# Kernel tuning notes

Hardware: AMD Instinct MI355X
Metric: run time of the kernel (lower is better)

Reference implementation:

```python
import jax, jax.numpy as jnp
import numpy as np

B, S, E, H = 2, 2048, 2048, 16
D = E // H  # 128


def setup_inputs() -> dict:
    key = jax.random.key(0)
    k0, k1, k2, k3 = jax.random.split(key, 4)
    x = jax.random.normal(k0, (B, S, E), dtype=jnp.float32)
    W_in = jax.random.normal(k1, (3 * E, E), dtype=jnp.float32) * 0.02
    b_in = jnp.zeros((3 * E,), dtype=jnp.float32)
    W_out = jax.random.normal(k2, (E, E), dtype=jnp.float32) * 0.02
    b_out = jnp.zeros((E,), dtype=jnp.float32)
    mask = jax.random.randint(k3, (B, S), 0, 2).astype(bool)  # True => masked out
    return {"x": x, "W_in": W_in, "b_in": b_in, "W_out": W_out, "b_out": b_out, "mask": mask}


def reference(x, W_in, b_in, W_out, b_out, mask):
    # fused QKV projection (torch Linear: y = x @ W^T + b)
    qkv = jnp.einsum('bse,fe->bsf', x, W_in) + b_in          # [B,S,3E]
    q, k, v = jnp.split(qkv, 3, axis=-1)
    q = q.reshape(B, S, H, D)
    k = k.reshape(B, S, H, D)
    v = v.reshape(B, S, H, D)
    scale = 1.0 / np.sqrt(D).astype(np.float32)
    scores = jnp.einsum('blhd,bshd->bhls', q, k) * scale     # [B,H,S,S]
    # 2D padding mask: True -> -inf additive bias, broadcast over heads/queries
    bias = jnp.where(mask[:, None, None, :], -jnp.inf, 0.0).astype(scores.dtype)
    attn = jax.nn.softmax(scores + bias, axis=-1)
    ctx = jnp.einsum('bhls,bshd->blhd', attn, v).reshape(B, S, E)
    out = jnp.einsum('ble,fe->blf', ctx, W_out) + b_out      # [B,S,E]
    return out
```

## Files before the change

kernel.cpp:

```cpp
#include <hip/hip_runtime.h>
#include <hip/hip_bf16.h>


typedef __bf16 bf16;
typedef __bf16 bf16x8 __attribute__((ext_vector_type(8)));
typedef __bf16 bf16x4 __attribute__((ext_vector_type(4)));
typedef float  f32x4  __attribute__((ext_vector_type(4)));
typedef float  f32x16 __attribute__((ext_vector_type(16)));

#define LOG2E 1.4426950408889634074f
#define SM_SCALE 0.08838834764831843f

#if defined(__has_builtin)
#if __has_builtin(__builtin_amdgcn_exp2f)
#define EXP2(x) __builtin_amdgcn_exp2f(x)
#else
#define EXP2(x) exp2f(x)
#endif
#else
#define EXP2(x) exp2f(x)
#endif

#define GLOAD_LDS16(gp, lp)                                                    \
  __builtin_amdgcn_global_load_lds(                                           \
      (__attribute__((address_space(1))) void*)(gp),                          \
      (__attribute__((address_space(3))) void*)(lp), 16, 0, 0)

__device__ inline unsigned int cvtpk_bf16(float lo, float hi) {
  unsigned int r;
  asm("v_cvt_pk_bf16_f32 %0, %1, %2" : "=v"(r) : "v"(lo), "v"(hi));
  return r;
}
__device__ inline void plane32_swap(unsigned int& a, unsigned int& b) {
  asm volatile("v_permlane32_swap_b32 %0, %1" : "+v"(a), "+v"(b));
}

__global__ void mask_bias_kernel(const unsigned char* __restrict__ mraw,
                                 float* __restrict__ kbias) {
  __shared__ int f1, f23, f84;
  if (threadIdx.x == 0) { f1 = 0; f23 = 0; f84 = 0; }
  __syncthreads();
  int a1 = 0, a23 = 0, a84 = 0;
  for (int i = threadIdx.x; i < 4096; i += blockDim.x) {
    unsigned char v = mraw[i];
    if (v) {
      int m4 = i & 3;
      if (m4 == 1) a1 = 1;
      else if (m4 >= 2) a23 = 1;
      else if ((i & 7) == 4) a84 = 1;
    }
  }
  if (a1) f1 = 1;
  if (a23) f23 = 1;
  if (a84) f84 = 1;
  __syncthreads();
  const bool isByte = (f1 != 0);
  const bool isF32 = !isByte && (f23 != 0);
  const bool isI32 = !isByte && !isF32 && (f84 != 0);
  for (int i = threadIdx.x; i < 4096; i += blockDim.x) {
    int m;
    if (isByte)      m = (mraw[i] != 0);
    else if (isF32)  m = (((const float*)mraw)[i] != 0.0f);
    else if (isI32)  m = (((const int*)mraw)[i] != 0);
    else             m = (((const long long*)mraw)[i] != 0LL);
    kbias[i] = m ? -30000.0f : 0.0f;
  }
}

__global__ void cvt_f32_bf16_kernel(const float* __restrict__ in,
                                    bf16* __restrict__ out, int n8) {
  int i = blockIdx.x * blockDim.x + threadIdx.x;
  if (i >= n8) return;
  const float4* p = (const float4*)in + (size_t)i * 2;
  float4 a = p[0], c = p[1];
  bf16x8 v;
  v[0] = (bf16)a.x; v[1] = (bf16)a.y; v[2] = (bf16)a.z; v[3] = (bf16)a.w;
  v[4] = (bf16)c.x; v[5] = (bf16)c.y; v[6] = (bf16)c.z; v[7] = (bf16)c.w;
  *((bf16x8*)out + i) = v;
}

template <int EPI>
__global__ __launch_bounds__(256, 2) void gemm_nt(
    const bf16* __restrict__ A, const bf16* __restrict__ B,
    const float* __restrict__ bias, void* __restrict__ Cout,
    bf16* __restrict__ vt, int M, int N, int K) {
  const int lane = threadIdx.x & 63;
  const int w = threadIdx.x >> 6;
  const int wr = w >> 1, wc = w & 1;
  const int l15 = lane & 15, lg = lane >> 4;

  const int nwg = gridDim.x;
  const int cpx = nwg >> 3;
  const int bid = blockIdx.x;
  const int swz = (bid & 7) * cpx + (bid >> 3);
  const int mtiles = M >> 7;
  const int mt = swz % mtiles, nt = swz / mtiles;
  const int m0 = mt << 7, n0 = nt << 7;

  __shared__ __align__(16) unsigned char smem[32768];
  unsigned char* sA = smem;
  unsigned char* sB = smem + 16384;

  const f32x4 Z4 = {0.f, 0.f, 0.f, 0.f};
  f32x4 acc[4][4];
#pragma unroll
  for (int i = 0; i < 4; i++)
#pragma unroll
    for (int j = 0; j < 4; j++) acc[i][j] = Z4;

  const int chunkbase = w * 1024 + lane * 16;

  for (int kt = 0; kt < K; kt += 64) {
#pragma unroll
    for (int c = 0; c < 4; c++) {
      int p = c * 4096 + chunkbase;
      int row = p >> 7, off = p & 127;
      int sb = off ^ ((row & 7) << 4);
      GLOAD_LDS16(A + (size_t)(m0 + row) * K + kt + (sb >> 1),
                  sA + c * 4096 + w * 1024);
      GLOAD_LDS16(B + (size_t)(n0 + row) * K + kt + (sb >> 1),
                  sB + c * 4096 + w * 1024);
    }
    __syncthreads();
#pragma unroll
    for (int ks = 0; ks < 2; ks++) {
      bf16x8 af[4], bfr[4];
#pragma unroll
      for (int i = 0; i < 4; i++) {
        int ar = wr * 64 + i * 16 + l15;
        af[i] = *(const bf16x8*)(sA + ar * 128 +
                                 ((ks * 64 + lg * 16) ^ ((ar & 7) << 4)));
        int br = wc * 64 + i * 16 + l15;
        bfr[i] = *(const bf16x8*)(sB + br * 128 +
                                  ((ks * 64 + lg * 16) ^ ((br & 7) << 4)));
      }
#pragma unroll
      for (int i = 0; i < 4; i++)
#pragma unroll
        for (int j = 0; j < 4; j++)
          acc[i][j] = __builtin_amdgcn_mfma_f32_16x16x32_bf16(
              af[i], bfr[j], acc[i][j], 0, 0, 0);
    }
    __syncthreads();
  }

#pragma unroll
  for (int i = 0; i < 4; i++) {
#pragma unroll
    for (int j = 0; j < 4; j++) {
      const int row0 = m0 + wr * 64 + i * 16 + lg * 4;
      const int col = n0 + wc * 64 + j * 16 + l15;
      const float bv = bias[col];
      f32x4 v = acc[i][j];
#pragma unroll
      for (int r = 0; r < 4; r++) v[r] += bv;
      if (EPI == 0) {
        float* Cf = (float*)Cout;
#pragma unroll
        for (int r = 0; r < 4; r++)
          Cf[(size_t)(row0 + r) * N + col] = v[r];
      } else {
        bf16* Cb = (bf16*)Cout;
        if (col < 4096) {
#pragma unroll
          for (int r = 0; r < 4; r++)
            Cb[(size_t)(row0 + r) * 6144 + col] = (bf16)v[r];
        } else {
          int dg = col - 4096;
          int hh = dg >> 7, dd = dg & 127;
          int bb = row0 >> 11, ss = row0 & 2047;
          bf16x4 pk;
#pragma unroll
          for (int r = 0; r < 4; r++) pk[r] = (bf16)v[r];
          *(bf16x4*)(vt + (size_t)((bb * 16 + hh) * 128 + dd) * 2048 + ss) = pk;
        }
      }
    }
  }
}

__global__ __launch_bounds__(512, 2) void attn_kernel(
    const bf16* __restrict__ qkv, const bf16* __restrict__ vt,
    const float* __restrict__ kbias, bf16* __restrict__ ctx) {
  const int tid = threadIdx.x;
  const int lane = tid & 63;
  const int w = tid >> 6;
  const int l31 = lane & 31;
  const int hb = lane >> 5;
  const int qt = blockIdx.x, h = blockIdx.y, b = blockIdx.z;

  __shared__ __align__(16) unsigned char smem[65536];

  const int qrow0 = qt * 256 + w * 32;
  const size_t tokbase = (size_t)b * 2048;
  const size_t vtbase = (size_t)((b * 16 + h) * 128) * 2048;
  const float* biasb = kbias + b * 2048;
  const float Cmul = SM_SCALE * LOG2E;

  auto stage = [&](int t, int bufsel) {
    const int kv0 = t * 64;
    unsigned char* base = smem + bufsel * 32768;
#pragma unroll
    for (int c = 0; c < 2; c++) {
      int p = c * 8192 + tid * 16;
      int rowk = p >> 8, offk = p & 255;
      int sbk = offk ^ ((rowk & 15) << 4);
      GLOAD_LDS16(qkv + (tokbase + kv0 + rowk) * 6144 + 2048 + h * 128 +
                      (sbk >> 1),
                  base + c * 8192 + w * 1024);
      int rowv = p >> 7, offv = p & 127;
      int sbv = offv ^ ((rowv & 7) << 4);
      GLOAD_LDS16(vt + vtbase + (size_t)rowv * 2048 + kv0 + (sbv >> 1),
                  base + 16384 + c * 8192 + w * 1024);
    }
  };

  stage(0, 0);

  bf16x8 qf[8];
#pragma unroll
  for (int ds = 0; ds < 8; ds++)
    qf[ds] = *(const bf16x8*)(qkv + (tokbase + qrow0 + l31) * 6144 + h * 128 +
                              ds * 16 + hb * 8);

  const f32x16 Z16 = {0.f, 0.f, 0.f, 0.f, 0.f, 0.f, 0.f, 0.f,
                      0.f, 0.f, 0.f, 0.f, 0.f, 0.f, 0.f, 0.f};
  f32x16 opv[4];
#pragma unroll
  for (int d0 = 0; d0 < 4; d0++) opv[d0] = Z16;
  float mrun = -15000.0f, lrun = 0.0f;

  __syncthreads();

  for (int t = 0; t < 32; t++) {
    const int buf = t & 1;
    const int kv0 = t * 64;
    if (t < 31) stage(t + 1, buf ^ 1);
    unsigned char* sK = smem + buf * 32768;
    unsigned char* sVT = sK + 16384;

    f32x4 bb[2][2][2];
#pragma unroll
    for (int kb = 0; kb < 2; kb++)
#pragma unroll
      for (int sb = 0; sb < 2; sb++)
#pragma unroll
        for (int g = 0; g < 2; g++)
          bb[kb][sb][g] = *(const f32x4*)(biasb + kv0 + kb * 32 + sb * 16 +
                                          g * 8 + 4 * hb);

    f32x16 accs[2];
    accs[0] = Z16; accs[1] = Z16;
    __builtin_amdgcn_s_setprio(1);
#pragma unroll
    for (int ds = 0; ds < 8; ds++) {
#pragma unroll
      for (int kb = 0; kb < 2; kb++) {
        int row = kb * 32 + l31;
        bf16x8 kf = *(const bf16x8*)(
            sK + row * 256 + ((ds * 32 + hb * 16) ^ ((row & 15) << 4)));
        accs[kb] = __builtin_amdgcn_mfma_f32_32x32x16_bf16(kf, qf[ds],
                                                           accs[kb], 0, 0, 0);
      }
    }
    __builtin_amdgcn_s_setprio(0);

#pragma unroll
    for (int kb = 0; kb < 2; kb++)
#pragma unroll
      for (int r = 0; r < 16; r++)
        accs[kb][r] =
            accs[kb][r] * Cmul + bb[kb][r >> 3][(r >> 2) & 1][r & 3];

    float vmax = accs[0][0];
#pragma unroll
    for (int kb = 0; kb < 2; kb++)
#pragma unroll
      for (int r = 0; r < 16; r++) vmax = fmaxf(vmax, accs[kb][r]);
    vmax = fmaxf(vmax, __shfl_xor(vmax, 32));

    if (__any(vmax > mrun + 8.0f)) {
      float mnew = fmaxf(mrun, vmax);
      float corr = EXP2(mrun - mnew);
      mrun = mnew;
      lrun *= corr;
#pragma unroll
      for (int r = 0; r < 16; r++) {
        float cv = __shfl(corr, (r & 3) + 8 * (r >> 2) + 4 * hb);
#pragma unroll
        for (int d0 = 0; d0 < 4; d0++) opv[d0][r] *= cv;
      }
    }

    float vsum = 0.0f;
#pragma unroll
    for (int kb = 0; kb < 2; kb++)
#pragma unroll
      for (int r = 0; r < 16; r++) {
        float p = EXP2(accs[kb][r] - mrun);
        accs[kb][r] = p;
        vsum += p;
      }
    vsum += __shfl_xor(vsum, 32);
    lrun += vsum;

    union { unsigned int w4[4]; bf16x8 v; } paf[4];
#pragma unroll
    for (int kb = 0; kb < 2; kb++)
#pragma unroll
      for (int sb = 0; sb < 2; sb++) {
        int r0 = sb * 8;
        unsigned int a0 = cvtpk_bf16(accs[kb][r0 + 0], accs[kb][r0 + 1]);
        unsigned int a1 = cvtpk_bf16(accs[kb][r0 + 2], accs[kb][r0 + 3]);
        unsigned int c0 = cvtpk_bf16(accs[kb][r0 + 4], accs[kb][r0 + 5]);
        unsigned int c1 = cvtpk_bf16(accs[kb][r0 + 6], accs[kb][r0 + 7]);
        plane32_swap(a0, c0);
        plane32_swap(a1, c1);
        int ks = kb * 2 + sb;
        paf[ks].w4[0] = a0; paf[ks].w4[1] = a1;
        paf[ks].w4[2] = c0; paf[ks].w4[3] = c1;
      }

    __builtin_amdgcn_s_setprio(1);
#pragma unroll
    for (int ks = 0; ks < 4; ks++) {
#pragma unroll
      for (int d0 = 0; d0 < 4; d0++) {
        int row = d0 * 32 + l31;
        bf16x8 vf = *(const bf16x8*)(
            sVT + row * 128 + ((ks * 32 + hb * 16) ^ ((row & 7) << 4)));
        opv[d0] = __builtin_amdgcn_mfma_f32_32x32x16_bf16(paf[ks].v, vf,
                                                          opv[d0], 0, 0, 0);
      }
    }
    __builtin_amdgcn_s_setprio(0);

    __syncthreads();
  }

  float linv = 1.0f / lrun;
#pragma unroll
  for (int r = 0; r < 16; r++) {
    float lv = __shfl(linv, (r & 3) + 8 * (r >> 2) + 4 * hb);
    int row = qrow0 + (r & 3) + 8 * (r >> 2) + 4 * hb;
#pragma unroll
    for (int d0 = 0; d0 < 4; d0++)
      ctx[(tokbase + row) * 2048 + h * 128 + d0 * 32 + l31] =
          (bf16)(opv[d0][r] * lv);
  }
}

extern "C" void kernel_launch(void* const* d_in, const int* in_sizes, int n_in,
                              void* d_out, int out_size, void* d_ws,
                              size_t ws_size, hipStream_t stream) {
  const float* x     = (const float*)d_in[0];
  const float* W_in  = (const float*)d_in[1];
  const float* b_in  = (const float*)d_in[2];
  const float* W_out = (const float*)d_in[3];
  const float* b_out = (const float*)d_in[4];
  const unsigned char* mask = (const unsigned char*)d_in[5];
  (void)in_sizes; (void)n_in; (void)out_size; (void)ws_size;

  char* ws = (char*)d_ws;
  bf16* xb    = (bf16*)(ws + 0);
  bf16* wib   = (bf16*)(ws + 16777216);
  bf16* wob   = (bf16*)(ws + 41943040);
  bf16* qkv   = (bf16*)(ws + 50331648);
  bf16* vt    = (bf16*)(ws + 100663296);
  bf16* ctx   = (bf16*)(ws + 117440512);
  float* kbias = (float*)(ws + 134217728);

  mask_bias_kernel<<<1, 1024, 0, stream>>>(mask, kbias);
  cvt_f32_bf16_kernel<<<4096, 256, 0, stream>>>(x, xb, 1048576);
  cvt_f32_bf16_kernel<<<6144, 256, 0, stream>>>(W_in, wib, 1572864);
  cvt_f32_bf16_kernel<<<2048, 256, 0, stream>>>(W_out, wob, 524288);
  gemm_nt<1><<<1536, 256, 0, stream>>>(xb, wib, b_in, (void*)qkv, vt, 4096,
                                       6144, 2048);
  attn_kernel<<<dim3(8, 16, 2), 512, 0, stream>>>(qkv, vt, kbias, ctx);
  gemm_nt<0><<<512, 256, 0, stream>>>(ctx, wob, b_out, d_out, (bf16*)nullptr,
                                      4096, 2048, 2048);
}
```

Measured before the change: 252.3 us.

## Add 256x256-tile QKV GEMM kernel with 8 waves and staged double buffering

Adds a new GEMM kernel for the QKV projection that uses 256x256 output tiles, 512 threads and a 128KB LDS double buffer. A and B tile loads are spread across the four sub-phases of each K step, with setprio raised around the MFMA blocks. Larger tiles raise data reuse per LDS load and cut global traffic. In exchange the grid shrinks to 384 workgroups on 256 CUs, which gives an uneven wave tail, and the large LDS footprint limits occupancy to one block per CU.

Result: slower. 270.8 us (+7.3%).

```diff
diff --git a/kernel.cpp b/kernel.cpp
--- a/kernel.cpp
+++ b/kernel.cpp
@@ -80,6 +80,158 @@
 }
 
 template <int EPI>
+__global__ __launch_bounds__(512, 2) void gemm256(
+    const bf16* __restrict__ A, const bf16* __restrict__ B,
+    const float* __restrict__ bias, void* __restrict__ Cout,
+    bf16* __restrict__ vt, int M, int N, int K) {
+  const int tid = threadIdx.x;
+  const int lane = tid & 63;
+  const int w = tid >> 6;
+  const int wm = w >> 2, wn = w & 3;
+  const int l15 = lane & 15, lg = lane >> 4;
+
+  const int nwg = gridDim.x;
+  const int cpx = nwg >> 3;
+  const int bid = blockIdx.x;
+  const int swz = (bid & 7) * cpx + (bid >> 3);
+  const int mtiles = M >> 8;
+  const int mt = swz % mtiles, ntl = swz / mtiles;
+  const int m0 = mt << 8, n0 = ntl << 8;
+
+  __shared__ __align__(16) unsigned char smem[131072];
+  const int NT = K >> 6;
+
+  auto stageA = [&](int t, int half) {
+    int base = (t & 1) * 32768 + half * 16384;
+#pragma unroll
+    for (int i = 0; i < 2; i++) {
+      int p = i * 8192 + tid * 16;
+      int row = p >> 7, off = p & 127;
+      int sb = off ^ ((row & 7) << 4);
+      GLOAD_LDS16(A + (size_t)(m0 + half * 128 + row) * K + t * 64 + (sb >> 1),
+                  smem + base + i * 8192 + w * 1024);
+    }
+  };
+  auto stageB = [&](int t, int half) {
+    int base = 65536 + (t & 1) * 32768 + half * 16384;
+#pragma unroll
+    for (int i = 0; i < 2; i++) {
+      int p = i * 8192 + tid * 16;
+      int row = p >> 7, off = p & 127;
+      int sb = off ^ ((row & 7) << 4);
+      GLOAD_LDS16(B + (size_t)(n0 + half * 128 + row) * K + t * 64 + (sb >> 1),
+                  smem + base + i * 8192 + w * 1024);
+    }
+  };
+
+  const f32x4 Z4 = {0.f, 0.f, 0.f, 0.f};
+  f32x4 acc[8][4];
+#pragma unroll
+  for (int i = 0; i < 8; i++)
+#pragma unroll
+    for (int j = 0; j < 4; j++) acc[i][j] = Z4;
+
+  stageA(0, 0); stageA(0, 1); stageB(0, 0); stageB(0, 1);
+  stageB(1, 0); stageB(1, 1);
+  asm volatile("s_waitcnt vmcnt(4)" ::: "memory");
+  __builtin_amdgcn_sched_barrier(0);
+  __builtin_amdgcn_s_barrier();
+
+  for (int t = 0; t < NT; t++) {
+    const int abase = (t & 1) * 32768;
+    const int bbase = 65536 + (t & 1) * 32768;
+    bf16x8 bfr[4][2];
+#pragma unroll
+    for (int p = 0; p < 4; p++) {
+      bf16x8 af[2][2];
+#pragma unroll
+      for (int i = 0; i < 2; i++) {
+        int ar = wm * 128 + (2 * p + i) * 16 + l15;
+#pragma unroll
+        for (int ks = 0; ks < 2; ks++)
+          af[i][ks] = *(const bf16x8*)(
+              smem + abase + ar * 128 + ((ks * 64 + lg * 16) ^ ((ar & 7) << 4)));
+      }
+      if (p == 0) {
+#pragma unroll
+        for (int nj = 0; nj < 4; nj++) {
+          int br = wn * 64 + nj * 16 + l15;
+#pragma unroll
+          for (int ks = 0; ks < 2; ks++)
+            bfr[nj][ks] = *(const bf16x8*)(
+                smem + bbase + br * 128 +
+                ((ks * 64 + lg * 16) ^ ((br & 7) << 4)));
+        }
+      }
+      if (p == 0 && t + 1 < NT) stageA(t + 1, 0);
+      if (p == 1 && t + 1 < NT) stageA(t + 1, 1);
+      if (p == 2 && t + 2 < NT) stageB(t + 2, 0);
+      if (p == 3 && t + 2 < NT) stageB(t + 2, 1);
+
+      __builtin_amdgcn_sched_barrier(0);
+      __builtin_amdgcn_s_barrier();
+      asm volatile("s_waitcnt lgkmcnt(0)" ::: "memory");
+      __builtin_amdgcn_sched_barrier(0);
+
+      __builtin_amdgcn_s_setprio(1);
+#pragma unroll
+      for (int i = 0; i < 2; i++)
+#pragma unroll
+        for (int nj = 0; nj < 4; nj++)
+#pragma unroll
+          for (int ks = 0; ks < 2; ks++)
+            acc[2 * p + i][nj] = __builtin_amdgcn_mfma_f32_16x16x32_bf16(
+                af[i][ks], bfr[nj][ks], acc[2 * p + i][nj], 0, 0, 0);
+      __builtin_amdgcn_s_setprio(0);
+
+      if (p == 3) {
+        if (t + 2 < NT) {
+          asm volatile("s_waitcnt vmcnt(4)" ::: "memory");
+        } else if (t + 1 < NT) {
+          asm volatile("s_waitcnt vmcnt(0)" ::: "memory");
+        }
+      }
+      __builtin_amdgcn_sched_barrier(0);
+      __builtin_amdgcn_s_barrier();
+    }
+  }
+
+#pragma unroll
+  for (int mi = 0; mi < 8; mi++) {
+#pragma unroll
+    for (int nj = 0; nj < 4; nj++) {
+      const int row0 = m0 + wm * 128 + mi * 16 + lg * 4;
+      const int col = n0 + wn * 64 + nj * 16 + l15;
+      const float bv = bias[col];
+      f32x4 v = acc[mi][nj];
+#pragma unroll
+      for (int r = 0; r < 4; r++) v[r] += bv;
+      if (EPI == 0) {
+        float* Cf = (float*)Cout;
+#pragma unroll
+        for (int r = 0; r < 4; r++)
+          Cf[(size_t)(row0 + r) * N + col] = v[r];
+      } else {
+        bf16* Cb = (bf16*)Cout;
+        if (col < 4096) {
+#pragma unroll
+          for (int r = 0; r < 4; r++)
+            Cb[(size_t)(row0 + r) * 6144 + col] = (bf16)v[r];
+        } else {
+          int dg = col - 4096;
+          int hh = dg >> 7, dd = dg & 127;
+          int bb = row0 >> 11, ss = row0 & 2047;
+          bf16x4 pk;
+#pragma unroll
+          for (int r = 0; r < 4; r++) pk[r] = (bf16)v[r];
+          *(bf16x4*)(vt + (size_t)((bb * 16 + hh) * 128 + dd) * 2048 + ss) = pk;
+        }
+      }
+    }
+  }
+}
+
+template <int EPI>
 __global__ __launch_bounds__(256, 2) void gemm_nt(
     const bf16* __restrict__ A, const bf16* __restrict__ B,
     const float* __restrict__ bias, void* __restrict__ Cout,
@@ -374,8 +526,8 @@
   cvt_f32_bf16_kernel<<<4096, 256, 0, stream>>>(x, xb, 1048576);
   cvt_f32_bf16_kernel<<<6144, 256, 0, stream>>>(W_in, wib, 1572864);
   cvt_f32_bf16_kernel<<<2048, 256, 0, stream>>>(W_out, wob, 524288);
-  gemm_nt<1><<<1536, 256, 0, stream>>>(xb, wib, b_in, (void*)qkv, vt, 4096,
-                                       6144, 2048);
+  gemm256<1><<<384, 512, 0, stream>>>(xb, wib, b_in, (void*)qkv, vt, 4096,
+                                      6144, 2048);
   attn_kernel<<<dim3(8, 16, 2), 512, 0, stream>>>(qkv, vt, kbias, ctx);
   gemm_nt<0><<<512, 256, 0, stream>>>(ctx, wob, b_out, d_out, (bf16*)nullptr,
                                       4096, 2048, 2048);
```

## Rewrite GEMM as 128x256 tile with multi-buffered async LDS pipeline

Applied to the files above, without the earlier changes.

Replaces the 128x128 single-buffered GEMM with a 512-thread, 128x256-tile kernel. A is double-buffered and B triple-buffered in a 128KB LDS region, and global-to-LDS loads for future k-steps are issued while MFMAs run. The work is split into two half-phases with explicit waitcnt, barriers and setprio to overlap memory with compute. The change is meant to hide load latency behind the synchronous load-then-compute loop and raise reuse per block. In exchange, 128KB of LDS limits occupancy to one block per CU, and the hand-tuned waitcnt counts are fragile.

Measured after the change: 258.3 us. 2.4% more time.

```diff
diff --git a/kernel.cpp b/kernel.cpp
--- a/kernel.cpp
+++ b/kernel.cpp
@@ -80,13 +80,14 @@
 }
 
 template <int EPI>
-__global__ __launch_bounds__(256, 2) void gemm_nt(
+__global__ __launch_bounds__(512, 2) void gemm_wide(
     const bf16* __restrict__ A, const bf16* __restrict__ B,
     const float* __restrict__ bias, void* __restrict__ Cout,
     bf16* __restrict__ vt, int M, int N, int K) {
-  const int lane = threadIdx.x & 63;
-  const int w = threadIdx.x >> 6;
-  const int wr = w >> 1, wc = w & 1;
+  const int tid = threadIdx.x;
+  const int lane = tid & 63;
+  const int w = tid >> 6;
+  const int wm = w >> 2, wn = w & 3;
   const int l15 = lane & 15, lg = lane >> 4;
 
   const int nwg = gridDim.x;
@@ -94,12 +95,34 @@
   const int bid = blockIdx.x;
   const int swz = (bid & 7) * cpx + (bid >> 3);
   const int mtiles = M >> 7;
-  const int mt = swz % mtiles, nt = swz / mtiles;
-  const int m0 = mt << 7, n0 = nt << 7;
-
-  __shared__ __align__(16) unsigned char smem[32768];
-  unsigned char* sA = smem;
-  unsigned char* sB = smem + 16384;
+  const int mt = swz % mtiles, ntl = swz / mtiles;
+  const int m0 = mt << 7, n0 = ntl << 8;
+
+  __shared__ __align__(16) unsigned char smem[131072];
+  const int NT = K >> 6;
+
+  auto stageA = [&](int t) {
+    int base = (t & 1) * 16384;
+#pragma unroll
+    for (int i = 0; i < 2; i++) {
+      int p = i * 8192 + tid * 16;
+      int row = p >> 7, off = p & 127;
+      int sb = off ^ ((row & 7) << 4);
+      GLOAD_LDS16(A + (size_t)(m0 + row) * K + t * 64 + (sb >> 1),
+                  smem + base + i * 8192 + w * 1024);
+    }
+  };
+  auto stageB2 = [&](int t, int i0) {
+    int base = 32768 + (t % 3) * 32768;
+#pragma unroll
+    for (int i = 0; i < 2; i++) {
+      int p = (i0 + i) * 8192 + tid * 16;
+      int row = p >> 7, off = p & 127;
+      int sb = off ^ ((row & 7) << 4);
+      GLOAD_LDS16(B + (size_t)(n0 + row) * K + t * 64 + (sb >> 1),
+                  smem + base + (i0 + i) * 8192 + w * 1024);
+    }
+  };
 
   const f32x4 Z4 = {0.f, 0.f, 0.f, 0.f};
   f32x4 acc[4][4];
@@ -108,50 +131,94 @@
 #pragma unroll
     for (int j = 0; j < 4; j++) acc[i][j] = Z4;
 
-  const int chunkbase = w * 1024 + lane * 16;
-
-  for (int kt = 0; kt < K; kt += 64) {
-#pragma unroll
-    for (int c = 0; c < 4; c++) {
-      int p = c * 4096 + chunkbase;
-      int row = p >> 7, off = p & 127;
-      int sb = off ^ ((row & 7) << 4);
-      GLOAD_LDS16(A + (size_t)(m0 + row) * K + kt + (sb >> 1),
-                  sA + c * 4096 + w * 1024);
-      GLOAD_LDS16(B + (size_t)(n0 + row) * K + kt + (sb >> 1),
-                  sB + c * 4096 + w * 1024);
-    }
-    __syncthreads();
-#pragma unroll
-    for (int ks = 0; ks < 2; ks++) {
-      bf16x8 af[4], bfr[4];
-#pragma unroll
-      for (int i = 0; i < 4; i++) {
-        int ar = wr * 64 + i * 16 + l15;
-        af[i] = *(const bf16x8*)(sA + ar * 128 +
-                                 ((ks * 64 + lg * 16) ^ ((ar & 7) << 4)));
-        int br = wc * 64 + i * 16 + l15;
-        bfr[i] = *(const bf16x8*)(sB + br * 128 +
-                                  ((ks * 64 + lg * 16) ^ ((br & 7) << 4)));
-      }
-#pragma unroll
-      for (int i = 0; i < 4; i++)
-#pragma unroll
-        for (int j = 0; j < 4; j++)
-          acc[i][j] = __builtin_amdgcn_mfma_f32_16x16x32_bf16(
-              af[i], bfr[j], acc[i][j], 0, 0, 0);
-    }
-    __syncthreads();
-  }
-
-#pragma unroll
-  for (int i = 0; i < 4; i++) {
-#pragma unroll
-    for (int j = 0; j < 4; j++) {
-      const int row0 = m0 + wr * 64 + i * 16 + lg * 4;
-      const int col = n0 + wc * 64 + j * 16 + l15;
+  stageA(0); stageB2(0, 0); stageB2(0, 2); stageB2(1, 0); stageB2(1, 2);
+  asm volatile("s_waitcnt vmcnt(4)" ::: "memory");
+  __builtin_amdgcn_sched_barrier(0);
+  __builtin_amdgcn_s_barrier();
+
+  for (int t = 0; t < NT; t++) {
+    const int abase = (t & 1) * 16384;
+    const int bbase = 32768 + (t % 3) * 32768;
+    bf16x8 bfr[4][2];
+
+    bf16x8 af0[2][2];
+#pragma unroll
+    for (int i = 0; i < 2; i++) {
+      int ar = wm * 64 + i * 16 + l15;
+#pragma unroll
+      for (int ks = 0; ks < 2; ks++)
+        af0[i][ks] = *(const bf16x8*)(
+            smem + abase + ar * 128 + ((ks * 64 + lg * 16) ^ ((ar & 7) << 4)));
+    }
+#pragma unroll
+    for (int nj = 0; nj < 4; nj++) {
+      int br = wn * 64 + nj * 16 + l15;
+#pragma unroll
+      for (int ks = 0; ks < 2; ks++)
+        bfr[nj][ks] = *(const bf16x8*)(
+            smem + bbase + br * 128 + ((ks * 64 + lg * 16) ^ ((br & 7) << 4)));
+    }
+    if (t + 1 < NT) stageA(t + 1);
+    if (t + 2 < NT) stageB2(t + 2, 0);
+    asm volatile("s_waitcnt lgkmcnt(8)" ::: "memory");
+    __builtin_amdgcn_sched_barrier(0);
+    __builtin_amdgcn_s_barrier();
+    asm volatile("s_waitcnt lgkmcnt(0)" ::: "memory");
+    __builtin_amdgcn_sched_barrier(0);
+    __builtin_amdgcn_s_setprio(1);
+#pragma unroll
+    for (int i = 0; i < 2; i++)
+#pragma unroll
+      for (int nj = 0; nj < 4; nj++)
+#pragma unroll
+        for (int ks = 0; ks < 2; ks++)
+          acc[i][nj] = __builtin_amdgcn_mfma_f32_16x16x32_bf16(
+              af0[i][ks], bfr[nj][ks], acc[i][nj], 0, 0, 0);
+    __builtin_amdgcn_s_setprio(0);
+    __builtin_amdgcn_sched_barrier(0);
+    __builtin_amdgcn_s_barrier();
+
+    bf16x8 af1[2][2];
+#pragma unroll
+    for (int i = 0; i < 2; i++) {
+      int ar = wm * 64 + (2 + i) * 16 + l15;
+#pragma unroll
+      for (int ks = 0; ks < 2; ks++)
+        af1[i][ks] = *(const bf16x8*)(
+            smem + abase + ar * 128 + ((ks * 64 + lg * 16) ^ ((ar & 7) << 4)));
+    }
+    if (t + 2 < NT) stageB2(t + 2, 2);
+    __builtin_amdgcn_sched_barrier(0);
+    __builtin_amdgcn_s_barrier();
+    asm volatile("s_waitcnt lgkmcnt(0)" ::: "memory");
+    __builtin_amdgcn_sched_barrier(0);
+    __builtin_amdgcn_s_setprio(1);
+#pragma unroll
+    for (int i = 0; i < 2; i++)
+#pragma unroll
+      for (int nj = 0; nj < 4; nj++)
+#pragma unroll
+        for (int ks = 0; ks < 2; ks++)
+          acc[2 + i][nj] = __builtin_amdgcn_mfma_f32_16x16x32_bf16(
+              af1[i][ks], bfr[nj][ks], acc[2 + i][nj], 0, 0, 0);
+    __builtin_amdgcn_s_setprio(0);
+    if (t + 2 < NT) {
+      asm volatile("s_waitcnt vmcnt(4)" ::: "memory");
+    } else if (t + 1 < NT) {
+      asm volatile("s_waitcnt vmcnt(0)" ::: "memory");
+    }
+    __builtin_amdgcn_sched_barrier(0);
+    __builtin_amdgcn_s_barrier();
+  }
+
+#pragma unroll
+  for (int mi = 0; mi < 4; mi++) {
+#pragma unroll
+    for (int nj = 0; nj < 4; nj++) {
+      const int row0 = m0 + wm * 64 + mi * 16 + lg * 4;
+      const int col = n0 + wn * 64 + nj * 16 + l15;
       const float bv = bias[col];
-      f32x4 v = acc[i][j];
+      f32x4 v = acc[mi][nj];
 #pragma unroll
       for (int r = 0; r < 4; r++) v[r] += bv;
       if (EPI == 0) {
@@ -374,9 +441,9 @@
   cvt_f32_bf16_kernel<<<4096, 256, 0, stream>>>(x, xb, 1048576);
   cvt_f32_bf16_kernel<<<6144, 256, 0, stream>>>(W_in, wib, 1572864);
   cvt_f32_bf16_kernel<<<2048, 256, 0, stream>>>(W_out, wob, 524288);
-  gemm_nt<1><<<1536, 256, 0, stream>>>(xb, wib, b_in, (void*)qkv, vt, 4096,
-                                       6144, 2048);
+  gemm_wide<1><<<768, 512, 0, stream>>>(xb, wib, b_in, (void*)qkv, vt, 4096,
+                                        6144, 2048);
   attn_kernel<<<dim3(8, 16, 2), 512, 0, stream>>>(qkv, vt, kbias, ctx);
-  gemm_nt<0><<<512, 256, 0, stream>>>(ctx, wob, b_out, d_out, (bf16*)nullptr,
-                                      4096, 2048, 2048);
-}
+  gemm_wide<0><<<256, 512, 0, stream>>>(ctx, wob, b_out, d_out, (bf16*)nullptr,
+                                        4096, 2048, 2048);
+}
```
